# Kernel optimization log

Measured on AMD Instinct MI355X. Metric: run time of the kernel, lower is better.

Reference implementation:

```python
import jax, jax.numpy as jnp
import numpy as np

N = 100000   # nodes
E = 640000   # directed edges
D = 128      # feature dim
C = 2        # classes


def setup_inputs() -> dict:
    key = jax.random.key(0)
    ks = jax.random.split(key, 7)
    s = 1.0 / np.sqrt(D)
    return {
        "x": jax.random.normal(ks[0], (N, D), jnp.float32),
        "edge_index": jax.random.randint(ks[1], (2, E), 0, N, jnp.int32),
        "W1": jax.random.normal(ks[2], (D, D), jnp.float32) * s,
        "b1": jnp.zeros((D,), jnp.float32),
        "W2": jax.random.normal(ks[3], (D, D), jnp.float32) * s,
        "b2": jnp.zeros((D,), jnp.float32),
        "Wfc": jax.random.normal(ks[4], (D, C), jnp.float32) * s,
        "bfc": jnp.zeros((C,), jnp.float32),
    }


def _gcn_conv(h, src, dst, W, b, n):
    """PyG GCNConv: y = D^{-1/2}(A+I)D^{-1/2} (h @ W) + b."""
    h = h @ W  # [N, D_out]
    loop = jnp.arange(n, dtype=src.dtype)
    s = jnp.concatenate([src, loop])
    d = jnp.concatenate([dst, loop])
    # degree of (A + I) counted at destination
    deg = jax.ops.segment_sum(jnp.ones_like(d, jnp.float32), d, num_segments=n)
    dinv = jax.lax.rsqrt(jnp.maximum(deg, 1.0))  # deg >= 1 via self loops
    norm = dinv[s] * dinv[d]                      # [E+N]
    msg = h[s] * norm[:, None]                    # gather + scale
    out = jax.ops.segment_sum(msg, d, num_segments=n)  # scatter-add
    return out + b


def reference(x, edge_index, W1, b1, W2, b2, Wfc, bfc):
    src, dst = edge_index[0], edge_index[1]
    n = x.shape[0]
    h = jax.nn.relu(_gcn_conv(x, src, dst, W1, b1, n))  # dropout = identity (eval)
    h = jax.nn.relu(_gcn_conv(h, src, dst, W2, b2, n))
    return h @ Wfc + bfc  # [N, 2] logits
```

## Files before the change

kernel.cpp:

```cpp
#include <hip/hip_runtime.h>
#include <hip/hip_bf16.h>

#define D 128
#define NBUCKET 64
#define BCAP 16384

typedef __bf16 bf16x8 __attribute__((ext_vector_type(8)));
typedef float f32x4 __attribute__((ext_vector_type(4)));


__global__ void prep_kernel(const float* __restrict__ W1, const float* __restrict__ W2,
                            __bf16* __restrict__ pw, int* __restrict__ bucket_cursor,
                            int* __restrict__ deghist) {
    int b = blockIdx.x;
    if (b < 128) {
        int t = b * 256 + threadIdx.x;
        int which = t >> 14, idx = t & 16383;
        const float* W = which ? W2 : W1;
        float w = W[idx];
        int k = idx >> 7, nn = idx & 127;
        int ks = which ? (((k & 15) << 3) | (k >> 4)) : k;
        int ntile = nn >> 4, nl = nn & 15;
        int kchunk = ks >> 5, quad = (ks >> 3) & 3, j = ks & 7;
        int o = (((ntile * 4 + kchunk) * 64 + quad * 16 + nl) << 3) + j;
        pw[(size_t)which * 16384 + o] = (__bf16)w;
    } else {
        int t = threadIdx.x;
        if (t < NBUCKET) bucket_cursor[t] = 0;
        else if (t < 128) deghist[t - 64] = 0;
    }
}

__global__ void mega1_kernel(const float* __restrict__ X, const __bf16* __restrict__ PW,
                             __bf16* __restrict__ Zs, int nrows, int gb,
                             const int* __restrict__ src, const int* __restrict__ dst,
                             int* __restrict__ bucket_cursor, int2* __restrict__ bucket_edges,
                             int e, int bucketW) {
    __shared__ __align__(16) char smem[32768];
    int t = threadIdx.x;
    int b = blockIdx.x;
    if (b >= gb) {
        int* hist = (int*)smem;
        int* gbase = hist + 64;
        if (t < NBUCKET) hist[t] = 0;
        __syncthreads();
        int i0 = ((b - gb) * 256 + t) * 4;
        int sv[4], dv[4], bk[4], ls[4];
        int nv = 0;
        if (i0 + 4 <= e) {
            int4 s4 = *(const int4*)(src + i0);
            int4 d4 = *(const int4*)(dst + i0);
            sv[0] = s4.x; sv[1] = s4.y; sv[2] = s4.z; sv[3] = s4.w;
            dv[0] = d4.x; dv[1] = d4.y; dv[2] = d4.z; dv[3] = d4.w;
            nv = 4;
        } else {
            for (int i = i0; i < e; i++) { sv[nv] = src[i]; dv[nv] = dst[i]; nv++; }
        }
        for (int u = 0; u < nv; u++) {
            bk[u] = dv[u] / bucketW;
            ls[u] = atomicAdd(&hist[bk[u]], 1);
        }
        __syncthreads();
        if (t < NBUCKET) gbase[t] = atomicAdd(&bucket_cursor[t], hist[t]);
        __syncthreads();
        for (int u = 0; u < nv; u++) {
            int pos = bk[u] * BCAP + gbase[bk[u]] + ls[u];
            bucket_edges[pos] = make_int2(sv[u], dv[u]);
        }
        return;
    }
    bf16x8* sB = (bf16x8*)smem;
    const bf16x8* PW8 = (const bf16x8*)PW;
#pragma unroll
    for (int i = 0; i < 8; i++) sB[t + 256 * i] = PW8[t + 256 * i];

    int wave = t >> 6, lane = t & 63;
    int qm = lane & 15, quad = lane >> 4;
    int r0 = b * 64 + wave * 16;
    int row = r0 + qm;
    bool valid = row < nrows;
    const float* xr = X + (size_t)row * D + quad * 8;

    bf16x8 ahi[4], alo[4];
#pragma unroll
    for (int c = 0; c < 4; c++) {
        float4 zf = {0.f, 0.f, 0.f, 0.f};
        float4 xa = valid ? ((const float4*)(xr + c * 32))[0] : zf;
        float4 xb = valid ? ((const float4*)(xr + c * 32))[1] : zf;
        float xs[8] = {xa.x, xa.y, xa.z, xa.w, xb.x, xb.y, xb.z, xb.w};
        bf16x8 h, l;
#pragma unroll
        for (int j = 0; j < 8; j++) {
            float v = xs[j];
            __bf16 hh = (__bf16)v;
            h[j] = hh;
            l[j] = (__bf16)(v - (float)hh);
        }
        ahi[c] = h; alo[c] = l;
    }

    f32x4 acc[8];
#pragma unroll
    for (int nt = 0; nt < 8; nt++) acc[nt] = (f32x4){0.f, 0.f, 0.f, 0.f};

    __syncthreads();

#pragma unroll
    for (int c = 0; c < 4; c++) {
#pragma unroll
        for (int nt = 0; nt < 8; nt++) {
            bf16x8 bb = sB[(nt * 4 + c) * 64 + lane];
            acc[nt] = __builtin_amdgcn_mfma_f32_16x16x32_bf16(ahi[c], bb, acc[nt], 0, 0, 0);
            acc[nt] = __builtin_amdgcn_mfma_f32_16x16x32_bf16(alo[c], bb, acc[nt], 0, 0, 0);
        }
    }

#pragma unroll
    for (int reg = 0; reg < 4; reg++) {
        int orow = r0 + quad * 4 + reg;
        if (orow < nrows) {
            bf16x8 o;
#pragma unroll
            for (int nt = 0; nt < 8; nt++) o[nt] = (__bf16)acc[nt][reg];
            *(bf16x8*)(Zs + (size_t)orow * D + qm * 8) = o;
        }
    }
}

__global__ void count2_kernel(const int2* __restrict__ bucket_edges,
                              const int* __restrict__ bucket_cursor,
                              int* __restrict__ counts, float* __restrict__ dinv,
                              int* __restrict__ partial, int* __restrict__ deghist,
                              int n, int bucketW, int subW) {
    __shared__ int bins[400];
    __shared__ int sm[256];
    __shared__ int hb[64];
    int b = blockIdx.x, t = threadIdx.x;
    int bk = b >> 2, j = b & 3;
    int ns = bk * bucketW + j * subW;
    int be = min((bk + 1) * bucketW, n);
    int ne = min(ns + subW, be);
    int w = ne - ns;
    if (w <= 0) { if (t == 0) partial[b] = 0; return; }
    for (int i = t; i < w; i += 256) bins[i] = 0;
    if (t < 64) hb[t] = 0;
    __syncthreads();
    int m = bucket_cursor[bk];
    const int2* eb = bucket_edges + (size_t)bk * BCAP;
    for (int i = t; i < m; i += 256) {
        int d = eb[i].y;
        if (d >= ns && d < ne) atomicAdd(&bins[d - ns], 1);
    }
    __syncthreads();
    int s = 0;
    for (int i = t; i < w; i += 256) {
        int c = bins[i];
        counts[ns + i] = c;
        dinv[ns + i] = rsqrtf((float)(c + 1));
        atomicAdd(&hb[min(c, 63)], 1);
        s += c;
    }
    sm[t] = s; __syncthreads();
    for (int off = 128; off > 0; off >>= 1) { if (t < off) sm[t] += sm[t + off]; __syncthreads(); }
    if (t == 0) partial[b] = sm[0];
    if (t < 64 && hb[t]) atomicAdd(&deghist[t], hb[t]);
}

__global__ void scan_top(int* partial, int* deghist, int* degcur, int nb) {
    __shared__ int sm[256];
    int t = threadIdx.x;
    int v = (t < nb) ? partial[t] : 0;
    sm[t] = v; __syncthreads();
    for (int off = 1; off < 256; off <<= 1) {
        int u = (t >= off) ? sm[t - off] : 0;
        __syncthreads();
        sm[t] += u;
        __syncthreads();
    }
    if (t < nb) partial[t] = sm[t] - v;
    __syncthreads();
    int d = (t < 64) ? deghist[t] : 0;
    sm[t] = d; __syncthreads();
    for (int off = 1; off < 64; off <<= 1) {
        int u = (t >= off && t < 64) ? sm[t - off] : 0;
        __syncthreads();
        if (t < 64) sm[t] += u;
        __syncthreads();
    }
    if (t < 64) degcur[t] = sm[t] - d;
}

__global__ void scanfill_kernel(const int2* __restrict__ bucket_edges,
                                const int* __restrict__ bucket_cursor,
                                const int* __restrict__ counts,
                                const int* __restrict__ partial,
                                int* __restrict__ row_ptr, int* __restrict__ csr,
                                int* __restrict__ degcur, int* __restrict__ order,
                                int n, int bucketW, int subW) {
    __shared__ int cur[400];
    __shared__ int sm[256];
    __shared__ int hb2[64];
    __shared__ int gb2[64];
    int b = blockIdx.x, t = threadIdx.x;
    int bk = b >> 2, j = b & 3;
    int ns = bk * bucketW + j * subW;
    int be = min((bk + 1) * bucketW, n);
    int ne = min(ns + subW, be);
    int w = ne - ns;
    if (w <= 0) return;
    if (t < 64) hb2[t] = 0;
    int i0 = t * 2;
    int c0 = (i0 < w) ? counts[ns + i0] : 0;
    int c1 = (i0 + 1 < w) ? counts[ns + i0 + 1] : 0;
    sm[t] = c0 + c1; __syncthreads();
    int own = c0 + c1;
    for (int off = 1; off < 256; off <<= 1) {
        int u = (t >= off) ? sm[t - off] : 0;
        __syncthreads();
        sm[t] += u;
        __syncthreads();
    }
    int base = partial[b] + sm[t] - own;
    if (i0 < w)     { row_ptr[ns + i0] = base;          cur[i0] = base; }
    if (i0 + 1 < w) { row_ptr[ns + i0 + 1] = base + c0; cur[i0 + 1] = base + c0; }
    int bin0 = min(c0, 63), bin1 = min(c1, 63);
    int r0 = (i0 < w) ? atomicAdd(&hb2[bin0], 1) : 0;
    int r1 = (i0 + 1 < w) ? atomicAdd(&hb2[bin1], 1) : 0;
    __syncthreads();
    if (t < 64 && hb2[t]) gb2[t] = atomicAdd(&degcur[t], hb2[t]);
    __syncthreads();
    if (i0 < w)     order[gb2[bin0] + r0] = ns + i0;
    if (i0 + 1 < w) order[gb2[bin1] + r1] = ns + i0 + 1;
    __syncthreads();
    int m = bucket_cursor[bk];
    const int2* eb = bucket_edges + (size_t)bk * BCAP;
    for (int i = t; i < m; i += 256) {
        int2 ed = eb[i];
        if (ed.y >= ns && ed.y < ne) {
            int pos = atomicAdd(&cur[ed.y - ns], 1);
            csr[pos] = ed.x;
        }
    }
}

__global__ void agg1_kernel(const __bf16* __restrict__ Zs, const int* __restrict__ row_ptr,
                            const int* __restrict__ counts, const int* __restrict__ csr,
                            const float* __restrict__ dinv, const float* __restrict__ bias,
                            const int* __restrict__ order, __bf16* __restrict__ Hs, int n) {
    int t = blockIdx.x * 256 + threadIdx.x;
    int idx = t >> 4, c = t & 15;
    if (idx >= n) return;
    int v = order[idx];
    float dv = dinv[v];
    const bf16x8* Z8 = (const bf16x8*)Zs;
    bf16x8 zc = Z8[(size_t)v * 16 + c];
    float sw = dv * dv;
    float acc[8];
#pragma unroll
    for (int j = 0; j < 8; j++) acc[j] = (float)zc[j] * sw;
    int start = row_ptr[v], cnt = counts[v];
    int i = 0;
    for (; i + 4 <= cnt; i += 4) {
        int s0 = csr[start + i], s1 = csr[start + i + 1];
        int s2 = csr[start + i + 2], s3 = csr[start + i + 3];
        bf16x8 m0 = Z8[(size_t)s0 * 16 + c];
        bf16x8 m1 = Z8[(size_t)s1 * 16 + c];
        bf16x8 m2 = Z8[(size_t)s2 * 16 + c];
        bf16x8 m3 = Z8[(size_t)s3 * 16 + c];
        float w0 = dinv[s0] * dv, w1 = dinv[s1] * dv;
        float w2 = dinv[s2] * dv, w3 = dinv[s3] * dv;
#pragma unroll
        for (int j = 0; j < 8; j++) acc[j] = fmaf(w0, (float)m0[j], acc[j]);
#pragma unroll
        for (int j = 0; j < 8; j++) acc[j] = fmaf(w1, (float)m1[j], acc[j]);
#pragma unroll
        for (int j = 0; j < 8; j++) acc[j] = fmaf(w2, (float)m2[j], acc[j]);
#pragma unroll
        for (int j = 0; j < 8; j++) acc[j] = fmaf(w3, (float)m3[j], acc[j]);
    }
    for (; i < cnt; i++) {
        int s0 = csr[start + i];
        float w0 = dinv[s0] * dv;
        bf16x8 m0 = Z8[(size_t)s0 * 16 + c];
#pragma unroll
        for (int j = 0; j < 8; j++) acc[j] = fmaf(w0, (float)m0[j], acc[j]);
    }
    bf16x8 o;
#pragma unroll
    for (int j = 0; j < 8; j++) o[j] = (__bf16)fmaxf(acc[j] + bias[j * 16 + c], 0.f);
    ((bf16x8*)Hs)[(size_t)v * 16 + c] = o;
}

__global__ void gemm2_mfma(const __bf16* __restrict__ Hs, const __bf16* __restrict__ PW,
                           __bf16* __restrict__ Zs, int nrows) {
    __shared__ bf16x8 sB[2048];
    int t = threadIdx.x;
    const bf16x8* PW8 = (const bf16x8*)PW;
#pragma unroll
    for (int i = 0; i < 8; i++) sB[t + 256 * i] = PW8[t + 256 * i];

    int wave = t >> 6, lane = t & 63;
    int qm = lane & 15, quad = lane >> 4;
    int r0 = blockIdx.x * 64 + wave * 16;
    int row = r0 + qm;
    bool valid = row < nrows;
    const __bf16* hr = Hs + (size_t)row * D + quad * 8;

    bf16x8 a[4];
#pragma unroll
    for (int c = 0; c < 4; c++) {
        bf16x8 z8 = {};
        a[c] = valid ? *(const bf16x8*)(hr + c * 32) : z8;
    }

    f32x4 acc[8];
#pragma unroll
    for (int nt = 0; nt < 8; nt++) acc[nt] = (f32x4){0.f, 0.f, 0.f, 0.f};

    __syncthreads();

#pragma unroll
    for (int c = 0; c < 4; c++) {
#pragma unroll
        for (int nt = 0; nt < 8; nt++) {
            bf16x8 b = sB[(nt * 4 + c) * 64 + lane];
            acc[nt] = __builtin_amdgcn_mfma_f32_16x16x32_bf16(a[c], b, acc[nt], 0, 0, 0);
        }
    }

#pragma unroll
    for (int reg = 0; reg < 4; reg++) {
        int orow = r0 + quad * 4 + reg;
        if (orow < nrows) {
            bf16x8 o;
#pragma unroll
            for (int nt = 0; nt < 8; nt++) o[nt] = (__bf16)acc[nt][reg];
            *(bf16x8*)(Zs + (size_t)orow * D + qm * 8) = o;
        }
    }
}

__global__ void agg2_fc_kernel(const __bf16* __restrict__ Zs, const int* __restrict__ row_ptr,
                               const int* __restrict__ counts, const int* __restrict__ csr,
                               const float* __restrict__ dinv, const float* __restrict__ bias,
                               const float* __restrict__ Wfc, const float* __restrict__ bfc,
                               const int* __restrict__ order, float* __restrict__ out, int n) {
    int t = blockIdx.x * 256 + threadIdx.x;
    int idx = t >> 4, c = t & 15;
    if (idx >= n) return;
    int v = order[idx];
    float dv = dinv[v];
    const bf16x8* Z8 = (const bf16x8*)Zs;
    bf16x8 zc = Z8[(size_t)v * 16 + c];
    float sw = dv * dv;
    float acc[8];
#pragma unroll
    for (int j = 0; j < 8; j++) acc[j] = (float)zc[j] * sw;
    int start = row_ptr[v], cnt = counts[v];
    int i = 0;
    for (; i + 4 <= cnt; i += 4) {
        int s0 = csr[start + i], s1 = csr[start + i + 1];
        int s2 = csr[start + i + 2], s3 = csr[start + i + 3];
        bf16x8 m0 = Z8[(size_t)s0 * 16 + c];
        bf16x8 m1 = Z8[(size_t)s1 * 16 + c];
        bf16x8 m2 = Z8[(size_t)s2 * 16 + c];
        bf16x8 m3 = Z8[(size_t)s3 * 16 + c];
        float w0 = dinv[s0] * dv, w1 = dinv[s1] * dv;
        float w2 = dinv[s2] * dv, w3 = dinv[s3] * dv;
#pragma unroll
        for (int j = 0; j < 8; j++) acc[j] = fmaf(w0, (float)m0[j], acc[j]);
#pragma unroll
        for (int j = 0; j < 8; j++) acc[j] = fmaf(w1, (float)m1[j], acc[j]);
#pragma unroll
        for (int j = 0; j < 8; j++) acc[j] = fmaf(w2, (float)m2[j], acc[j]);
#pragma unroll
        for (int j = 0; j < 8; j++) acc[j] = fmaf(w3, (float)m3[j], acc[j]);
    }
    for (; i < cnt; i++) {
        int s0 = csr[start + i];
        float w0 = dinv[s0] * dv;
        bf16x8 m0 = Z8[(size_t)s0 * 16 + c];
#pragma unroll
        for (int j = 0; j < 8; j++) acc[j] = fmaf(w0, (float)m0[j], acc[j]);
    }
    float a0 = 0.f, a1 = 0.f;
#pragma unroll
    for (int j = 0; j < 8; j++) {
        int p = j * 16 + c;
        float hj = fmaxf(acc[j] + bias[p], 0.f);
        a0 = fmaf(hj, Wfc[p * 2], a0);
        a1 = fmaf(hj, Wfc[p * 2 + 1], a1);
    }
#pragma unroll
    for (int off = 8; off > 0; off >>= 1) {
        a0 += __shfl_down(a0, off, 16);
        a1 += __shfl_down(a1, off, 16);
    }
    if (c == 0) {
        out[(size_t)v * 2 + 0] = a0 + bfc[0];
        out[(size_t)v * 2 + 1] = a1 + bfc[1];
    }
}


extern "C" void kernel_launch(void* const* d_in, const int* in_sizes, int n_in,
                              void* d_out, int out_size, void* d_ws, size_t ws_size,
                              hipStream_t stream) {
    const float* x   = (const float*)d_in[0];
    const int*   ei  = (const int*)d_in[1];
    const float* W1  = (const float*)d_in[2];
    const float* b1  = (const float*)d_in[3];
    const float* W2  = (const float*)d_in[4];
    const float* b2  = (const float*)d_in[5];
    const float* Wfc = (const float*)d_in[6];
    const float* bfc = (const float*)d_in[7];
    float* out = (float*)d_out;

    int n = in_sizes[0] / D;
    int e = in_sizes[1] / 2;
    const int* src = ei;
    const int* dst = ei + e;

    int bucketW = (n + NBUCKET - 1) / NBUCKET;
    int subW = (bucketW + 3) / 4;

    char* ws = (char*)d_ws;
    size_t nb = (size_t)n * 4;
    int*    counts  = (int*)(ws);
    float*  dinv    = (float*)(ws + nb);
    int*    rowptr  = (int*)(ws + 2 * nb);
    int*    partial = (int*)(ws + 3 * nb);
    int*    bcur    = (int*)(ws + 3 * nb + 1024);
    int*    deghist = (int*)(ws + 3 * nb + 1280);
    int*    degcur  = (int*)(ws + 3 * nb + 1536);
    int*    order   = (int*)(ws + 3 * nb + 2048);
    int2*   bedges  = (int2*)(ws + 4 * nb + 2048);
    size_t  off1    = 4 * nb + 2048 + (size_t)NBUCKET * BCAP * 8;
    int*    csr     = (int*)(ws + off1);
    __bf16* pw      = (__bf16*)(ws + off1 + (size_t)e * 4);
    __bf16* z1      = (__bf16*)(ws + off1 + (size_t)e * 4 + 65536);
    __bf16* h1      = z1 + (size_t)n * D;
    __bf16* z2      = h1 + (size_t)n * D;

    int eab = ((e + 3) / 4 + 255) / 256;
    int gb  = (n + 63) / 64;
    int ab  = ((n * 16) + 255) / 256;

    prep_kernel<<<129, 256, 0, stream>>>(W1, W2, pw, bcur, deghist);
    mega1_kernel<<<gb + eab, 256, 0, stream>>>(x, pw, z1, n, gb, src, dst,
                                               bcur, bedges, e, bucketW);
    count2_kernel<<<256, 256, 0, stream>>>(bedges, bcur, counts, dinv, partial, deghist,
                                           n, bucketW, subW);
    scan_top<<<1, 256, 0, stream>>>(partial, deghist, degcur, 256);
    scanfill_kernel<<<256, 256, 0, stream>>>(bedges, bcur, counts, partial, rowptr, csr,
                                             degcur, order, n, bucketW, subW);
    agg1_kernel<<<ab, 256, 0, stream>>>(z1, rowptr, counts, csr, dinv, b1, order, h1, n);
    gemm2_mfma<<<gb, 256, 0, stream>>>(h1, pw + 16384, z2, n);
    agg2_fc_kernel<<<ab, 256, 0, stream>>>(z2, rowptr, counts, csr, dinv, b2, Wfc, bfc,
                                           order, out, n);
}
```

Baseline: 238.8 us.

## Fuse layer-1 aggregation with layer-2 GEMM and prescale Z2 by dinv

Layer-1 aggregation and the second MFMA GEMM now run in one kernel. Each block aggregates 64 degree-ordered nodes into a swizzled shared-memory tile and multiplies that tile by W2, so the H1 intermediate no longer makes a round trip through global memory. The GEMM output is scaled by dinv of the source node, which lets agg2 drop the per-edge dinv gather and multiply and apply dv once at the end. In exchange, fewer threads per block do the aggregation (4 rows each), the shared-memory footprint grows, and Z2 writes are scattered by the order permutation.

```diff
diff --git a/kernel.cpp b/kernel.cpp
--- a/kernel.cpp
+++ b/kernel.cpp
@@ -243,99 +243,107 @@
     }
 }
 
-__global__ void agg1_kernel(const __bf16* __restrict__ Zs, const int* __restrict__ row_ptr,
-                            const int* __restrict__ counts, const int* __restrict__ csr,
-                            const float* __restrict__ dinv, const float* __restrict__ bias,
-                            const int* __restrict__ order, __bf16* __restrict__ Hs, int n) {
-    int t = blockIdx.x * 256 + threadIdx.x;
-    int idx = t >> 4, c = t & 15;
-    if (idx >= n) return;
-    int v = order[idx];
-    float dv = dinv[v];
-    const bf16x8* Z8 = (const bf16x8*)Zs;
-    bf16x8 zc = Z8[(size_t)v * 16 + c];
-    float sw = dv * dv;
-    float acc[8];
-#pragma unroll
-    for (int j = 0; j < 8; j++) acc[j] = (float)zc[j] * sw;
-    int start = row_ptr[v], cnt = counts[v];
-    int i = 0;
-    for (; i + 4 <= cnt; i += 4) {
-        int s0 = csr[start + i], s1 = csr[start + i + 1];
-        int s2 = csr[start + i + 2], s3 = csr[start + i + 3];
-        bf16x8 m0 = Z8[(size_t)s0 * 16 + c];
-        bf16x8 m1 = Z8[(size_t)s1 * 16 + c];
-        bf16x8 m2 = Z8[(size_t)s2 * 16 + c];
-        bf16x8 m3 = Z8[(size_t)s3 * 16 + c];
-        float w0 = dinv[s0] * dv, w1 = dinv[s1] * dv;
-        float w2 = dinv[s2] * dv, w3 = dinv[s3] * dv;
-#pragma unroll
-        for (int j = 0; j < 8; j++) acc[j] = fmaf(w0, (float)m0[j], acc[j]);
-#pragma unroll
-        for (int j = 0; j < 8; j++) acc[j] = fmaf(w1, (float)m1[j], acc[j]);
-#pragma unroll
-        for (int j = 0; j < 8; j++) acc[j] = fmaf(w2, (float)m2[j], acc[j]);
-#pragma unroll
-        for (int j = 0; j < 8; j++) acc[j] = fmaf(w3, (float)m3[j], acc[j]);
-    }
-    for (; i < cnt; i++) {
-        int s0 = csr[start + i];
-        float w0 = dinv[s0] * dv;
-        bf16x8 m0 = Z8[(size_t)s0 * 16 + c];
-#pragma unroll
-        for (int j = 0; j < 8; j++) acc[j] = fmaf(w0, (float)m0[j], acc[j]);
-    }
-    bf16x8 o;
-#pragma unroll
-    for (int j = 0; j < 8; j++) o[j] = (__bf16)fmaxf(acc[j] + bias[j * 16 + c], 0.f);
-    ((bf16x8*)Hs)[(size_t)v * 16 + c] = o;
-}
-
-__global__ void gemm2_mfma(const __bf16* __restrict__ Hs, const __bf16* __restrict__ PW,
-                           __bf16* __restrict__ Zs, int nrows) {
+__global__ void agg1_gemm2_kernel(const __bf16* __restrict__ Zs, const int* __restrict__ row_ptr,
+                                  const int* __restrict__ counts, const int* __restrict__ csr,
+                                  const float* __restrict__ dinv, const float* __restrict__ bias,
+                                  const __bf16* __restrict__ PW, const int* __restrict__ order,
+                                  __bf16* __restrict__ Z2, int n) {
+    __shared__ __align__(16) __bf16 sH[64 * 128];
     __shared__ bf16x8 sB[2048];
     int t = threadIdx.x;
     const bf16x8* PW8 = (const bf16x8*)PW;
 #pragma unroll
     for (int i = 0; i < 8; i++) sB[t + 256 * i] = PW8[t + 256 * i];
 
+    int gbase = blockIdx.x * 64;
+    int grp = t >> 4, c = t & 15;
+
+    float bs[8];
+#pragma unroll
+    for (int j = 0; j < 8; j++) bs[j] = bias[j * 16 + c];
+
+    const bf16x8* Z8 = (const bf16x8*)Zs;
+    for (int r = 0; r < 4; r++) {
+        int lr = r * 16 + grp;
+        int idx = gbase + lr;
+        bf16x8 o = {};
+        if (idx < n) {
+            int v = order[idx];
+            float dv = dinv[v];
+            bf16x8 zc = Z8[(size_t)v * 16 + c];
+            float sw = dv * dv;
+            float acc[8];
+#pragma unroll
+            for (int j = 0; j < 8; j++) acc[j] = (float)zc[j] * sw;
+            int start = row_ptr[v], cnt = counts[v];
+            int i = 0;
+            for (; i + 4 <= cnt; i += 4) {
+                int s0 = csr[start + i], s1 = csr[start + i + 1];
+                int s2 = csr[start + i + 2], s3 = csr[start + i + 3];
+                bf16x8 m0 = Z8[(size_t)s0 * 16 + c];
+                bf16x8 m1 = Z8[(size_t)s1 * 16 + c];
+                bf16x8 m2 = Z8[(size_t)s2 * 16 + c];
+                bf16x8 m3 = Z8[(size_t)s3 * 16 + c];
+                float w0 = dinv[s0] * dv, w1 = dinv[s1] * dv;
+                float w2 = dinv[s2] * dv, w3 = dinv[s3] * dv;
+#pragma unroll
+                for (int j = 0; j < 8; j++) acc[j] = fmaf(w0, (float)m0[j], acc[j]);
+#pragma unroll
+                for (int j = 0; j < 8; j++) acc[j] = fmaf(w1, (float)m1[j], acc[j]);
+#pragma unroll
+                for (int j = 0; j < 8; j++) acc[j] = fmaf(w2, (float)m2[j], acc[j]);
+#pragma unroll
+                for (int j = 0; j < 8; j++) acc[j] = fmaf(w3, (float)m3[j], acc[j]);
+            }
+            for (; i < cnt; i++) {
+                int s0 = csr[start + i];
+                float w0 = dinv[s0] * dv;
+                bf16x8 m0 = Z8[(size_t)s0 * 16 + c];
+#pragma unroll
+                for (int j = 0; j < 8; j++) acc[j] = fmaf(w0, (float)m0[j], acc[j]);
+            }
+#pragma unroll
+            for (int j = 0; j < 8; j++) o[j] = (__bf16)fmaxf(acc[j] + bs[j], 0.f);
+        }
+        *(bf16x8*)(sH + lr * 128 + ((c ^ (lr & 7)) << 3)) = o;
+    }
+    __syncthreads();
+
     int wave = t >> 6, lane = t & 63;
     int qm = lane & 15, quad = lane >> 4;
-    int r0 = blockIdx.x * 64 + wave * 16;
-    int row = r0 + qm;
-    bool valid = row < nrows;
-    const __bf16* hr = Hs + (size_t)row * D + quad * 8;
+    int lrow = wave * 16 + qm;
 
     bf16x8 a[4];
 #pragma unroll
-    for (int c = 0; c < 4; c++) {
-        bf16x8 z8 = {};
-        a[c] = valid ? *(const bf16x8*)(hr + c * 32) : z8;
+    for (int cc = 0; cc < 4; cc++) {
+        int slot = quad + cc * 4;
+        a[cc] = *(const bf16x8*)(sH + lrow * 128 + ((slot ^ (lrow & 7)) << 3));
     }
 
     f32x4 acc[8];
 #pragma unroll
     for (int nt = 0; nt < 8; nt++) acc[nt] = (f32x4){0.f, 0.f, 0.f, 0.f};
 
-    __syncthreads();
-
-#pragma unroll
-    for (int c = 0; c < 4; c++) {
+#pragma unroll
+    for (int cc = 0; cc < 4; cc++) {
 #pragma unroll
         for (int nt = 0; nt < 8; nt++) {
-            bf16x8 b = sB[(nt * 4 + c) * 64 + lane];
-            acc[nt] = __builtin_amdgcn_mfma_f32_16x16x32_bf16(a[c], b, acc[nt], 0, 0, 0);
+            bf16x8 bb = sB[(nt * 4 + cc) * 64 + lane];
+            acc[nt] = __builtin_amdgcn_mfma_f32_16x16x32_bf16(a[cc], bb, acc[nt], 0, 0, 0);
         }
     }
 
 #pragma unroll
     for (int reg = 0; reg < 4; reg++) {
-        int orow = r0 + quad * 4 + reg;
-        if (orow < nrows) {
+        int lrr = wave * 16 + quad * 4 + reg;
+        int gidx = gbase + lrr;
+        if (gidx < n) {
+            int v = order[gidx];
+            float sc = dinv[v];
             bf16x8 o;
 #pragma unroll
-            for (int nt = 0; nt < 8; nt++) o[nt] = (__bf16)acc[nt][reg];
-            *(bf16x8*)(Zs + (size_t)orow * D + qm * 8) = o;
+            for (int nt = 0; nt < 8; nt++) o[nt] = (__bf16)(acc[nt][reg] * sc);
+            *(bf16x8*)(Z2 + (size_t)v * D + qm * 8) = o;
         }
     }
 }
@@ -352,10 +360,9 @@
     float dv = dinv[v];
     const bf16x8* Z8 = (const bf16x8*)Zs;
     bf16x8 zc = Z8[(size_t)v * 16 + c];
-    float sw = dv * dv;
     float acc[8];
 #pragma unroll
-    for (int j = 0; j < 8; j++) acc[j] = (float)zc[j] * sw;
+    for (int j = 0; j < 8; j++) acc[j] = (float)zc[j];
     int start = row_ptr[v], cnt = counts[v];
     int i = 0;
     for (; i + 4 <= cnt; i += 4) {
@@ -365,29 +372,26 @@
         bf16x8 m1 = Z8[(size_t)s1 * 16 + c];
         bf16x8 m2 = Z8[(size_t)s2 * 16 + c];
         bf16x8 m3 = Z8[(size_t)s3 * 16 + c];
-        float w0 = dinv[s0] * dv, w1 = dinv[s1] * dv;
-        float w2 = dinv[s2] * dv, w3 = dinv[s3] * dv;
-#pragma unroll
-        for (int j = 0; j < 8; j++) acc[j] = fmaf(w0, (float)m0[j], acc[j]);
-#pragma unroll
-        for (int j = 0; j < 8; j++) acc[j] = fmaf(w1, (float)m1[j], acc[j]);
-#pragma unroll
-        for (int j = 0; j < 8; j++) acc[j] = fmaf(w2, (float)m2[j], acc[j]);
-#pragma unroll
-        for (int j = 0; j < 8; j++) acc[j] = fmaf(w3, (float)m3[j], acc[j]);
+#pragma unroll
+        for (int j = 0; j < 8; j++) acc[j] += (float)m0[j];
+#pragma unroll
+        for (int j = 0; j < 8; j++) acc[j] += (float)m1[j];
+#pragma unroll
+        for (int j = 0; j < 8; j++) acc[j] += (float)m2[j];
+#pragma unroll
+        for (int j = 0; j < 8; j++) acc[j] += (float)m3[j];
     }
     for (; i < cnt; i++) {
         int s0 = csr[start + i];
-        float w0 = dinv[s0] * dv;
         bf16x8 m0 = Z8[(size_t)s0 * 16 + c];
 #pragma unroll
-        for (int j = 0; j < 8; j++) acc[j] = fmaf(w0, (float)m0[j], acc[j]);
+        for (int j = 0; j < 8; j++) acc[j] += (float)m0[j];
     }
     float a0 = 0.f, a1 = 0.f;
 #pragma unroll
     for (int j = 0; j < 8; j++) {
         int p = j * 16 + c;
-        float hj = fmaxf(acc[j] + bias[p], 0.f);
+        float hj = fmaxf(fmaf(dv, acc[j], bias[p]), 0.f);
         a0 = fmaf(hj, Wfc[p * 2], a0);
         a1 = fmaf(hj, Wfc[p * 2 + 1], a1);
     }
@@ -439,8 +443,7 @@
     int*    csr     = (int*)(ws + off1);
     __bf16* pw      = (__bf16*)(ws + off1 + (size_t)e * 4);
     __bf16* z1      = (__bf16*)(ws + off1 + (size_t)e * 4 + 65536);
-    __bf16* h1      = z1 + (size_t)n * D;
-    __bf16* z2      = h1 + (size_t)n * D;
+    __bf16* z2      = z1 + (size_t)n * D;
 
     int eab = ((e + 3) / 4 + 255) / 256;
     int gb  = (n + 63) / 64;
@@ -454,8 +457,8 @@
     scan_top<<<1, 256, 0, stream>>>(partial, deghist, degcur, 256);
     scanfill_kernel<<<256, 256, 0, stream>>>(bedges, bcur, counts, partial, rowptr, csr,
                                              degcur, order, n, bucketW, subW);
-    agg1_kernel<<<ab, 256, 0, stream>>>(z1, rowptr, counts, csr, dinv, b1, order, h1, n);
-    gemm2_mfma<<<gb, 256, 0, stream>>>(h1, pw + 16384, z2, n);
+    agg1_gemm2_kernel<<<gb, 256, 0, stream>>>(z1, rowptr, counts, csr, dinv, b1,
+                                              pw + 16384, order, z2, n);
     agg2_fc_kernel<<<ab, 256, 0, stream>>>(z2, rowptr, counts, csr, dinv, b2, Wfc, bfc,
                                            order, out, n);
 }
```

Result: slower. 247.4 us (+3.6%).
